# Kernel tuning notes

Hardware: AMD Instinct MI355X
Metric: run time of the kernel (lower is better)

The kernel has to match this reference:

```python
import jax, jax.numpy as jnp
import numpy as np

N_NODES = 50000
N_EDGES = 800000
D = 64
K_ORDER = 8


def setup_inputs() -> dict:
    key = jax.random.key(0)
    k1, k2, k3, k4 = jax.random.split(key, 4)
    x = jax.random.normal(k1, (N_NODES, D), dtype=jnp.float32)
    edge_index = jax.random.randint(k2, (2, N_EDGES), 0, N_NODES, dtype=jnp.int64)
    edge_weight = jax.random.uniform(k3, (N_EDGES,), dtype=jnp.float32)
    weight = jax.random.normal(k4, (K_ORDER, D, D), dtype=jnp.float32) * 0.05
    bias = jnp.zeros((D,), dtype=jnp.float32)
    return {"x": x, "edge_index": edge_index, "edge_weight": edge_weight,
            "weight": weight, "bias": bias}


def _propagate(h, src, dst, edge_weight, n_nodes):
    # sparse matvec: out[i] = sum_{e: dst_e = i} w_e * h[src_e]
    msgs = edge_weight[:, None] * h[src]          # (E, D)
    return jax.ops.segment_sum(msgs, dst, num_segments=n_nodes)


def reference(x, edge_index, edge_weight, weight, bias):
    src, dst = edge_index[0], edge_index[1]
    n = x.shape[0]
    K = weight.shape[0]
    # Chebyshev recursion: T_0 = x, T_1 = L x, T_k = 2 L T_{k-1} - T_{k-2}
    Tx_prev = x                                   # T_0
    out = jnp.einsum('nd,de->ne', Tx_prev, weight[0])
    Tx_cur = _propagate(x, src, dst, edge_weight, n)  # T_1
    if K > 1:
        out = out + jnp.einsum('nd,de->ne', Tx_cur, weight[1])
    for k in range(2, K):
        Tx_next = 2.0 * _propagate(Tx_cur, src, dst, edge_weight, n) - Tx_prev
        out = out + jnp.einsum('nd,de->ne', Tx_next, weight[k])
        Tx_prev, Tx_cur = Tx_cur, Tx_next
    return out + bias
```

## Files before the change

kernel.cpp:

```cpp
#include <hip/hip_runtime.h>
#include <hip/hip_fp16.h>

#define DD  64
#define BKT 256
#define CAP 4608
#define CHK 4096


__device__ __forceinline__ unsigned pk_bf16(float a, float b) {
    unsigned ua = __float_as_uint(a), ub = __float_as_uint(b);
    ua = (ua + 0x7fffu + ((ua >> 16) & 1u)) >> 16;
    ub = (ub + 0x7fffu + ((ub >> 16) & 1u)) & 0xffff0000u;
    return (ua & 0xffffu) | ub;
}
__device__ __forceinline__ void unpk_bf16(unsigned u, float& lo, float& hi) {
    lo = __uint_as_float(u << 16);
    hi = __uint_as_float(u & 0xffff0000u);
}


__global__ __launch_bounds__(256) void p1fill_kernel(
    const int* __restrict__ ei, const float* __restrict__ ew,
    int* __restrict__ bcur, uint2* __restrict__ tmp, int E)
{
    __shared__ int lh[256], gb[256], lc[256];
    int tid = threadIdx.x;
    lh[tid] = 0;
    __syncthreads();
    int base = blockIdx.x * CHK;
#pragma unroll
    for (int j = 0; j < CHK / 256; ++j) {
        int e = base + j * 256 + tid;
        if (e < E) atomicAdd(&lh[ei[E + e] >> 8], 1);
    }
    __syncthreads();
    {
        gb[tid] = lh[tid] ? atomicAdd(&bcur[tid], lh[tid]) : 0;
        lc[tid] = 0;
    }
    __syncthreads();
#pragma unroll
    for (int j = 0; j < CHK / 256; ++j) {
        int e = base + j * 256 + tid;
        if (e < E) {
            int src = ei[e], dst = ei[E + e];
            unsigned short hw = __half_as_ushort(__float2half(ew[e]));
            unsigned rec = (unsigned)(unsigned short)src | ((unsigned)hw << 16);
            int b = dst >> 8;
            int pos = gb[b] + atomicAdd(&lc[b], 1);
            if (pos < CAP)
                tmp[(size_t)b * CAP + pos] = make_uint2(rec, (unsigned)(dst & 255));
        }
    }
}

__global__ __launch_bounds__(256) void p1scan_kernel(
    const int* __restrict__ bcur, int* __restrict__ bptr, int NB, int E)
{
    __shared__ int s[256];
    int t = threadIdx.x;
    int v = (t < NB) ? min(bcur[t], CAP) : 0;
    s[t] = v;
    __syncthreads();
    for (int off = 1; off < 256; off <<= 1) {
        int u = (t >= off) ? s[t - off] : 0;
        __syncthreads();
        s[t] += u;
        __syncthreads();
    }
    if (t < NB) bptr[t] = s[t] - v;
    if (t == 0) bptr[NB] = (NB > 0) ? s[255] : E;
}

__global__ __launch_bounds__(1024) void p2sort_kernel(
    const uint2* __restrict__ tmp, const int* __restrict__ bcur,
    const int* __restrict__ bptr, unsigned* __restrict__ edges,
    int* __restrict__ row_ptr, int N, int E, int NB)
{
    __shared__ int lh[BKT], lx[BKT], lc[BKT];
    __shared__ unsigned lout[CAP];
    int b = blockIdx.x;
    size_t tbase = (size_t)b * CAP;
    int obase = bptr[b];
    int cnt = min(bcur[b], CAP);
    int t = threadIdx.x;
    if (t < BKT) lh[t] = 0;
    __syncthreads();
    for (int i = t; i < cnt; i += 1024)
        atomicAdd(&lh[tmp[tbase + i].y & 255], 1);
    __syncthreads();
    if (t < BKT) { lc[t] = lh[t]; lx[t] = lh[t]; }
    __syncthreads();
    for (int off = 1; off < BKT; off <<= 1) {
        int v = 0;
        if (t < BKT && t >= off) v = lx[t - off];
        __syncthreads();
        if (t < BKT && t >= off) lx[t] += v;
        __syncthreads();
    }
    if (t < BKT) { lx[t] -= lc[t]; lc[t] = 0; }
    __syncthreads();
    for (int i = t; i < cnt; i += 1024) {
        uint2 r = tmp[tbase + i];
        int dl = r.y & 255;
        int pos = lx[dl] + atomicAdd(&lc[dl], 1);
        lout[pos] = r.x;
    }
    __syncthreads();
    for (int i = t; i < cnt; i += 1024) edges[obase + i] = lout[i];
    if (t < BKT) {
        int d = b * BKT + t;
        if (d < N) row_ptr[d] = obase + lx[t];
    }
    if (b == NB - 1 && t == 0) row_ptr[N] = E;
}

__global__ __launch_bounds__(256) void quant_kernel(
    const float4* __restrict__ src, uint4* __restrict__ dst, int n8)
{
    int i = blockIdx.x * 256 + threadIdx.x;
    if (i >= n8) return;
    float4 a = src[2 * i], b = src[2 * i + 1];
    dst[i] = make_uint4(pk_bf16(a.x, a.y), pk_bf16(a.z, a.w),
                        pk_bf16(b.x, b.y), pk_bf16(b.z, b.w));
}

__global__ __launch_bounds__(256) void prop_kernel(
    const unsigned short* __restrict__ h, const unsigned short* __restrict__ prev,
    const unsigned* __restrict__ edges, const int* __restrict__ row_ptr,
    unsigned short* __restrict__ Tnext, int N)
{
    int lane = threadIdx.x & 63;
    int wid  = (blockIdx.x * 256 + threadIdx.x) >> 6;
    int n0 = wid * 2, n1 = n0 + 1;
    if (n0 >= N) return;
    bool v1 = n1 < N;

    int g  = lane >> 3;
    int c8 = (lane & 7) << 3;

    int beg0 = row_ptr[n0];
    int end0 = row_ptr[n0 + 1];
    int beg1 = end0;
    int end1 = v1 ? row_ptr[n1 + 1] : end0;

    float4 A0 = make_float4(0.f, 0.f, 0.f, 0.f), A1 = A0;
    float4 B0 = A0, B1 = A0;

    int b0 = beg0, b1 = beg1;
    while (b0 < end0 || b1 < end1) {
        unsigned RA0 = (b0 + g     < end0) ? __builtin_nontemporal_load(edges + b0 + g)     : 0u;
        unsigned RB0 = (b0 + 8 + g < end0) ? __builtin_nontemporal_load(edges + b0 + 8 + g) : 0u;
        unsigned RA1 = (b1 + g     < end1) ? __builtin_nontemporal_load(edges + b1 + g)     : 0u;
        unsigned RB1 = (b1 + 8 + g < end1) ? __builtin_nontemporal_load(edges + b1 + 8 + g) : 0u;
        float wa0 = __half2float(__ushort_as_half((unsigned short)(RA0 >> 16)));
        float wb0 = __half2float(__ushort_as_half((unsigned short)(RB0 >> 16)));
        float wa1 = __half2float(__ushort_as_half((unsigned short)(RA1 >> 16)));
        float wb1 = __half2float(__ushort_as_half((unsigned short)(RB1 >> 16)));
        const uint4 va0 = *reinterpret_cast<const uint4*>(
            &h[(size_t)(RA0 & 0xffffu) * DD + c8]);
        const uint4 vb0 = *reinterpret_cast<const uint4*>(
            &h[(size_t)(RB0 & 0xffffu) * DD + c8]);
        const uint4 va1 = *reinterpret_cast<const uint4*>(
            &h[(size_t)(RA1 & 0xffffu) * DD + c8]);
        const uint4 vb1 = *reinterpret_cast<const uint4*>(
            &h[(size_t)(RB1 & 0xffffu) * DD + c8]);
        float lo, hi;
        unpk_bf16(va0.x, lo, hi); A0.x = fmaf(wa0, lo, A0.x); A0.y = fmaf(wa0, hi, A0.y);
        unpk_bf16(va0.y, lo, hi); A0.z = fmaf(wa0, lo, A0.z); A0.w = fmaf(wa0, hi, A0.w);
        unpk_bf16(va0.z, lo, hi); A1.x = fmaf(wa0, lo, A1.x); A1.y = fmaf(wa0, hi, A1.y);
        unpk_bf16(va0.w, lo, hi); A1.z = fmaf(wa0, lo, A1.z); A1.w = fmaf(wa0, hi, A1.w);
        unpk_bf16(vb0.x, lo, hi); A0.x = fmaf(wb0, lo, A0.x); A0.y = fmaf(wb0, hi, A0.y);
        unpk_bf16(vb0.y, lo, hi); A0.z = fmaf(wb0, lo, A0.z); A0.w = fmaf(wb0, hi, A0.w);
        unpk_bf16(vb0.z, lo, hi); A1.x = fmaf(wb0, lo, A1.x); A1.y = fmaf(wb0, hi, A1.y);
        unpk_bf16(vb0.w, lo, hi); A1.z = fmaf(wb0, lo, A1.z); A1.w = fmaf(wb0, hi, A1.w);
        unpk_bf16(va1.x, lo, hi); B0.x = fmaf(wa1, lo, B0.x); B0.y = fmaf(wa1, hi, B0.y);
        unpk_bf16(va1.y, lo, hi); B0.z = fmaf(wa1, lo, B0.z); B0.w = fmaf(wa1, hi, B0.w);
        unpk_bf16(va1.z, lo, hi); B1.x = fmaf(wa1, lo, B1.x); B1.y = fmaf(wa1, hi, B1.y);
        unpk_bf16(va1.w, lo, hi); B1.z = fmaf(wa1, lo, B1.z); B1.w = fmaf(wa1, hi, B1.w);
        unpk_bf16(vb1.x, lo, hi); B0.x = fmaf(wb1, lo, B0.x); B0.y = fmaf(wb1, hi, B0.y);
        unpk_bf16(vb1.y, lo, hi); B0.z = fmaf(wb1, lo, B0.z); B0.w = fmaf(wb1, hi, B0.w);
        unpk_bf16(vb1.z, lo, hi); B1.x = fmaf(wb1, lo, B1.x); B1.y = fmaf(wb1, hi, B1.y);
        unpk_bf16(vb1.w, lo, hi); B1.z = fmaf(wb1, lo, B1.z); B1.w = fmaf(wb1, hi, B1.w);
        b0 += 16; b1 += 16;
    }

#pragma unroll
    for (int mk = 8; mk <= 32; mk <<= 1) {
        A0.x += __shfl_xor(A0.x, mk); A0.y += __shfl_xor(A0.y, mk);
        A0.z += __shfl_xor(A0.z, mk); A0.w += __shfl_xor(A0.w, mk);
        A1.x += __shfl_xor(A1.x, mk); A1.y += __shfl_xor(A1.y, mk);
        A1.z += __shfl_xor(A1.z, mk); A1.w += __shfl_xor(A1.w, mk);
        B0.x += __shfl_xor(B0.x, mk); B0.y += __shfl_xor(B0.y, mk);
        B0.z += __shfl_xor(B0.z, mk); B0.w += __shfl_xor(B0.w, mk);
        B1.x += __shfl_xor(B1.x, mk); B1.y += __shfl_xor(B1.y, mk);
        B1.z += __shfl_xor(B1.z, mk); B1.w += __shfl_xor(B1.w, mk);
    }

    if (prev) {
        {
            const uint4 p = *reinterpret_cast<const uint4*>(&prev[(size_t)n0 * DD + c8]);
            float lo, hi;
            unpk_bf16(p.x, lo, hi); A0.x = 2.f * A0.x - lo; A0.y = 2.f * A0.y - hi;
            unpk_bf16(p.y, lo, hi); A0.z = 2.f * A0.z - lo; A0.w = 2.f * A0.w - hi;
            unpk_bf16(p.z, lo, hi); A1.x = 2.f * A1.x - lo; A1.y = 2.f * A1.y - hi;
            unpk_bf16(p.w, lo, hi); A1.z = 2.f * A1.z - lo; A1.w = 2.f * A1.w - hi;
        }
        if (v1) {
            const uint4 p = *reinterpret_cast<const uint4*>(&prev[(size_t)n1 * DD + c8]);
            float lo, hi;
            unpk_bf16(p.x, lo, hi); B0.x = 2.f * B0.x - lo; B0.y = 2.f * B0.y - hi;
            unpk_bf16(p.y, lo, hi); B0.z = 2.f * B0.z - lo; B0.w = 2.f * B0.w - hi;
            unpk_bf16(p.z, lo, hi); B1.x = 2.f * B1.x - lo; B1.y = 2.f * B1.y - hi;
            unpk_bf16(p.w, lo, hi); B1.z = 2.f * B1.z - lo; B1.w = 2.f * B1.w - hi;
        }
    }
    if (g == 0) {
        *reinterpret_cast<uint4*>(&Tnext[(size_t)n0 * DD + c8]) =
            make_uint4(pk_bf16(A0.x, A0.y), pk_bf16(A0.z, A0.w),
                       pk_bf16(A1.x, A1.y), pk_bf16(A1.z, A1.w));
        if (v1)
            *reinterpret_cast<uint4*>(&Tnext[(size_t)n1 * DD + c8]) =
                make_uint4(pk_bf16(B0.x, B0.y), pk_bf16(B0.z, B0.w),
                           pk_bf16(B1.x, B1.y), pk_bf16(B1.z, B1.w));
    }
}

__global__ __launch_bounds__(256) void mega_gemm_kernel(
    const unsigned short* __restrict__ T0, const unsigned short* __restrict__ T1,
    const unsigned short* __restrict__ T2, const unsigned short* __restrict__ T3,
    const float* __restrict__ W, const float* __restrict__ bias,
    float* __restrict__ out, int N, int nord, int init)
{
    __shared__ float Ws[DD * DD];
    __shared__ float Ts[32][68];
    const unsigned short* Tl[4] = { T0, T1, T2, T3 };

    int nb0 = blockIdx.x * 32;
    int tid = threadIdx.x;
    int r = tid >> 4, c = tid & 15;
    int r2 = r * 2, c4 = c * 4;

    float acc[2][4];
    if (init) {
        const float4 bb = *reinterpret_cast<const float4*>(&bias[c4]);
#pragma unroll
        for (int i = 0; i < 2; ++i) {
            acc[i][0] = bb.x; acc[i][1] = bb.y; acc[i][2] = bb.z; acc[i][3] = bb.w;
        }
    } else {
#pragma unroll
        for (int i = 0; i < 2; ++i)
            acc[i][0] = acc[i][1] = acc[i][2] = acc[i][3] = 0.f;
    }

    int nl = tid >> 3, q = tid & 7;
    bool tvalid = (nb0 + nl) < N;

    uint4 tv = make_uint4(0, 0, 0, 0);
    float wv[16];
    if (tvalid)
        tv = *reinterpret_cast<const uint4*>(&Tl[0][(size_t)(nb0 + nl) * DD + q * 8]);
#pragma unroll
    for (int j = 0; j < 16; ++j) wv[j] = W[tid + j * 256];

    for (int kc = 0; kc < nord; ++kc) {
        __syncthreads();
        {
            float f0, f1, f2, f3, f4, f5, f6, f7;
            unpk_bf16(tv.x, f0, f1); unpk_bf16(tv.y, f2, f3);
            unpk_bf16(tv.z, f4, f5); unpk_bf16(tv.w, f6, f7);
            *reinterpret_cast<float4*>(&Ts[nl][q * 8])     = make_float4(f0, f1, f2, f3);
            *reinterpret_cast<float4*>(&Ts[nl][q * 8 + 4]) = make_float4(f4, f5, f6, f7);
#pragma unroll
            for (int j = 0; j < 16; ++j) Ws[tid + j * 256] = wv[j];
        }
        __syncthreads();

        if (kc + 1 < nord) {
            if (tvalid)
                tv = *reinterpret_cast<const uint4*>(
                    &Tl[kc + 1][(size_t)(nb0 + nl) * DD + q * 8]);
            const float* Wn = W + (size_t)(kc + 1) * DD * DD;
#pragma unroll
            for (int j = 0; j < 16; ++j) wv[j] = Wn[tid + j * 256];
        }

#pragma unroll 8
        for (int d = 0; d < DD; ++d) {
            float a0 = Ts[r2 + 0][d], a1 = Ts[r2 + 1][d];
            float4 b = *reinterpret_cast<const float4*>(&Ws[d * DD + c4]);
            acc[0][0] = fmaf(a0, b.x, acc[0][0]); acc[0][1] = fmaf(a0, b.y, acc[0][1]);
            acc[0][2] = fmaf(a0, b.z, acc[0][2]); acc[0][3] = fmaf(a0, b.w, acc[0][3]);
            acc[1][0] = fmaf(a1, b.x, acc[1][0]); acc[1][1] = fmaf(a1, b.y, acc[1][1]);
            acc[1][2] = fmaf(a1, b.z, acc[1][2]); acc[1][3] = fmaf(a1, b.w, acc[1][3]);
        }
    }

#pragma unroll
    for (int i = 0; i < 2; ++i) {
        int n = nb0 + r2 + i;
        if (n < N) {
            float4 o = make_float4(acc[i][0], acc[i][1], acc[i][2], acc[i][3]);
            if (!init) {
                float4 p = *reinterpret_cast<const float4*>(&out[(size_t)n * DD + c4]);
                o.x += p.x; o.y += p.y; o.z += p.z; o.w += p.w;
            }
            *reinterpret_cast<float4*>(&out[(size_t)n * DD + c4]) = o;
        }
    }
}


static inline size_t rup(size_t x) { return (x + 255) & ~(size_t)255; }

extern "C" void kernel_launch(void* const* d_in, const int* in_sizes, int n_in,
                              void* d_out, int out_size, void* d_ws, size_t ws_size,
                              hipStream_t stream) {
    const float* x    = (const float*)d_in[0];
    const int*   ei   = (const int*)  d_in[1];
    const float* ew   = (const float*)d_in[2];
    const float* W    = (const float*)d_in[3];
    const float* bias = (const float*)d_in[4];
    float* out = (float*)d_out;

    int N = in_sizes[0] / DD;
    int E = in_sizes[2];
    int K = in_sizes[3] / (DD * DD);
    int NB = (N + BKT - 1) / BKT;

    size_t nb_bf = (size_t)N * DD * sizeof(unsigned short);

    char* w = (char*)d_ws;
    unsigned short* B[5];
    for (int i = 0; i < 5; ++i) { B[i] = (unsigned short*)w; w += rup(nb_bf); }
    unsigned* edges  = (unsigned*)w;  w += rup((size_t)E * sizeof(unsigned));
    int* row_ptr = (int*)w;           w += rup((size_t)(N + 1) * sizeof(int));
    int* bptr    = (int*)w;           w += rup((size_t)(NB + 1) * sizeof(int));
    int* bcur    = (int*)w;           w += rup((size_t)NB * sizeof(int));
    uint2* tmp   = (uint2*)B[1];

    int pb   = (N + 7) / 8;
    int gb32 = (N + 31) / 32;
    int n8   = (N * DD) / 8;
    int qb   = (n8 + 255) / 256;
    int fb   = (E + CHK - 1) / CHK;

    hipMemsetAsync(bcur, 0, (size_t)NB * sizeof(int), stream);
    p1fill_kernel<<<fb, 256, 0, stream>>>(ei, ew, bcur, tmp, E);
    p1scan_kernel<<<1, 256, 0, stream>>>(bcur, bptr, NB, E);
    p2sort_kernel<<<NB, 1024, 0, stream>>>(tmp, bcur, bptr, edges, row_ptr, N, E, NB);

    quant_kernel<<<qb, 256, 0, stream>>>((const float4*)x, (uint4*)B[0], n8);

    int done = 0;
    for (int k = 1; k < K; ++k) {
        const unsigned short* cur  = B[(k - 1) % 5];
        const unsigned short* prev = (k >= 2) ? B[(k - 2) % 5] : nullptr;
        unsigned short*       nxt  = B[k % 5];
        prop_kernel<<<pb, 256, 0, stream>>>(cur, prev, edges, row_ptr, nxt, N);
        if (k % 4 == 3) {
            int c0 = done;
            mega_gemm_kernel<<<gb32, 256, 0, stream>>>(
                B[(c0 + 0) % 5], B[(c0 + 1) % 5], B[(c0 + 2) % 5], B[(c0 + 3) % 5],
                W + (size_t)c0 * DD * DD, bias, out, N, 4, done == 0);
            done += 4;
        }
    }
    if (done < K) {
        mega_gemm_kernel<<<gb32, 256, 0, stream>>>(
            B[(done + 0) % 5], B[(done + 1) % 5],
            B[(done + 2) % 5], B[(done + 3) % 5],
            W + (size_t)done * DD * DD, bias, out, N, K - done, done == 0);
    }
}
```

Measured before the change: 255.0 us.

## Replace FP32 FMA Chebyshev GEMM with bf16 MFMA using split hi/lo weights

Rewrites the fused per-order output GEMM to use 16x16x32 bf16 MFMA instructions instead of scalar FP32 FMAs over shared-memory tiles. Each block now handles 64 nodes, one 16-row tile per wavefront. The bf16 activations are fed directly from global memory as the A operand. Weights are split in shared memory into bf16 high and low parts, each multiplied separately, to keep near-FP32 weight precision. The change cuts ALU and LDS traffic in the GEMM stage. In exchange it doubles the MFMA count, re-converts the weights in every block for every order, and reads the last partial tile without a bounds check.

Measured after the change: 234.7 us. 8.0% less time.

```diff
diff --git a/kernel.cpp b/kernel.cpp
--- a/kernel.cpp
+++ b/kernel.cpp
@@ -5,6 +5,9 @@
 #define BKT 256
 #define CAP 4608
 #define CHK 4096
+
+typedef __attribute__((ext_vector_type(8))) short bf16x8;
+typedef __attribute__((ext_vector_type(4))) float f32x4;
 
 
 __device__ __forceinline__ unsigned pk_bf16(float a, float b) {
@@ -16,6 +19,13 @@
 __device__ __forceinline__ void unpk_bf16(unsigned u, float& lo, float& hi) {
     lo = __uint_as_float(u << 16);
     hi = __uint_as_float(u & 0xffff0000u);
+}
+__device__ __forceinline__ unsigned short bf16_rtn(float f) {
+    unsigned u = __float_as_uint(f);
+    return (unsigned short)((u + 0x7fffu + ((u >> 16) & 1u)) >> 16);
+}
+__device__ __forceinline__ float bf16_to_f(unsigned short h) {
+    return __uint_as_float((unsigned)h << 16);
 }
 
 
@@ -226,87 +236,74 @@
     }
 }
 
-__global__ __launch_bounds__(256) void mega_gemm_kernel(
+__global__ __launch_bounds__(256) void mega_mfma_kernel(
     const unsigned short* __restrict__ T0, const unsigned short* __restrict__ T1,
     const unsigned short* __restrict__ T2, const unsigned short* __restrict__ T3,
     const float* __restrict__ W, const float* __restrict__ bias,
     float* __restrict__ out, int N, int nord, int init)
 {
-    __shared__ float Ws[DD * DD];
-    __shared__ float Ts[32][68];
+    __shared__ unsigned short WtHi[64][72];
+    __shared__ unsigned short WtLo[64][72];
     const unsigned short* Tl[4] = { T0, T1, T2, T3 };
 
-    int nb0 = blockIdx.x * 32;
-    int tid = threadIdx.x;
-    int r = tid >> 4, c = tid & 15;
-    int r2 = r * 2, c4 = c * 4;
-
-    float acc[2][4];
-    if (init) {
-        const float4 bb = *reinterpret_cast<const float4*>(&bias[c4]);
-#pragma unroll
-        for (int i = 0; i < 2; ++i) {
-            acc[i][0] = bb.x; acc[i][1] = bb.y; acc[i][2] = bb.z; acc[i][3] = bb.w;
-        }
-    } else {
-#pragma unroll
-        for (int i = 0; i < 2; ++i)
-            acc[i][0] = acc[i][1] = acc[i][2] = acc[i][3] = 0.f;
-    }
-
-    int nl = tid >> 3, q = tid & 7;
-    bool tvalid = (nb0 + nl) < N;
-
-    uint4 tv = make_uint4(0, 0, 0, 0);
-    float wv[16];
-    if (tvalid)
-        tv = *reinterpret_cast<const uint4*>(&Tl[0][(size_t)(nb0 + nl) * DD + q * 8]);
-#pragma unroll
-    for (int j = 0; j < 16; ++j) wv[j] = W[tid + j * 256];
+    int tid  = threadIdx.x;
+    int lane = tid & 63;
+    int wv   = tid >> 6;
+    int nb0  = blockIdx.x * 64;
+    int l15  = lane & 15;
+    int lg   = lane >> 4;
+
+    f32x4 acc[4];
+#pragma unroll
+    for (int t = 0; t < 4; ++t) acc[t] = (f32x4){0.f, 0.f, 0.f, 0.f};
 
     for (int kc = 0; kc < nord; ++kc) {
         __syncthreads();
         {
-            float f0, f1, f2, f3, f4, f5, f6, f7;
-            unpk_bf16(tv.x, f0, f1); unpk_bf16(tv.y, f2, f3);
-            unpk_bf16(tv.z, f4, f5); unpk_bf16(tv.w, f6, f7);
-            *reinterpret_cast<float4*>(&Ts[nl][q * 8])     = make_float4(f0, f1, f2, f3);
-            *reinterpret_cast<float4*>(&Ts[nl][q * 8 + 4]) = make_float4(f4, f5, f6, f7);
-#pragma unroll
-            for (int j = 0; j < 16; ++j) Ws[tid + j * 256] = wv[j];
-        }
-        __syncthreads();
-
-        if (kc + 1 < nord) {
-            if (tvalid)
-                tv = *reinterpret_cast<const uint4*>(
-                    &Tl[kc + 1][(size_t)(nb0 + nl) * DD + q * 8]);
-            const float* Wn = W + (size_t)(kc + 1) * DD * DD;
-#pragma unroll
-            for (int j = 0; j < 16; ++j) wv[j] = Wn[tid + j * 256];
-        }
-
-#pragma unroll 8
-        for (int d = 0; d < DD; ++d) {
-            float a0 = Ts[r2 + 0][d], a1 = Ts[r2 + 1][d];
-            float4 b = *reinterpret_cast<const float4*>(&Ws[d * DD + c4]);
-            acc[0][0] = fmaf(a0, b.x, acc[0][0]); acc[0][1] = fmaf(a0, b.y, acc[0][1]);
-            acc[0][2] = fmaf(a0, b.z, acc[0][2]); acc[0][3] = fmaf(a0, b.w, acc[0][3]);
-            acc[1][0] = fmaf(a1, b.x, acc[1][0]); acc[1][1] = fmaf(a1, b.y, acc[1][1]);
-            acc[1][2] = fmaf(a1, b.z, acc[1][2]); acc[1][3] = fmaf(a1, b.w, acc[1][3]);
-        }
-    }
-
-#pragma unroll
-    for (int i = 0; i < 2; ++i) {
-        int n = nb0 + r2 + i;
-        if (n < N) {
-            float4 o = make_float4(acc[i][0], acc[i][1], acc[i][2], acc[i][3]);
-            if (!init) {
-                float4 p = *reinterpret_cast<const float4*>(&out[(size_t)n * DD + c4]);
-                o.x += p.x; o.y += p.y; o.z += p.z; o.w += p.w;
+            const float* Wk = W + (size_t)kc * DD * DD;
+            int d = tid >> 2, c0 = (tid & 3) * 16;
+#pragma unroll
+            for (int j = 0; j < 16; ++j) {
+                float w = Wk[d * DD + c0 + j];
+                unsigned short hi = bf16_rtn(w);
+                unsigned short lo = bf16_rtn(w - bf16_to_f(hi));
+                WtHi[c0 + j][d] = hi;
+                WtLo[c0 + j][d] = lo;
             }
-            *reinterpret_cast<float4*>(&out[(size_t)n * DD + c4]) = o;
+        }
+        __syncthreads();
+
+        const unsigned short* Tk = Tl[kc];
+        size_t abase = (size_t)(nb0 + wv * 16 + l15) * DD + lg * 8;
+        bf16x8 a0 = *reinterpret_cast<const bf16x8*>(&Tk[abase]);
+        bf16x8 a1 = *reinterpret_cast<const bf16x8*>(&Tk[abase + 32]);
+
+#pragma unroll
+        for (int kch = 0; kch < 2; ++kch) {
+            bf16x8 a = kch ? a1 : a0;
+            int kb = kch * 32 + lg * 8;
+#pragma unroll
+            for (int t = 0; t < 4; ++t) {
+                bf16x8 bhi = *reinterpret_cast<const bf16x8*>(&WtHi[t * 16 + l15][kb]);
+                bf16x8 blo = *reinterpret_cast<const bf16x8*>(&WtLo[t * 16 + l15][kb]);
+                acc[t] = __builtin_amdgcn_mfma_f32_16x16x32_bf16(a, bhi, acc[t], 0, 0, 0);
+                acc[t] = __builtin_amdgcn_mfma_f32_16x16x32_bf16(a, blo, acc[t], 0, 0, 0);
+            }
+        }
+    }
+
+#pragma unroll
+    for (int t = 0; t < 4; ++t) {
+        int col = t * 16 + l15;
+        float bv = init ? bias[col] : 0.f;
+#pragma unroll
+        for (int j = 0; j < 4; ++j) {
+            int n = nb0 + wv * 16 + lg * 4 + j;
+            if (n < N) {
+                float v = acc[t][j] + bv;
+                if (!init) v += out[(size_t)n * DD + col];
+                out[(size_t)n * DD + col] = v;
+            }
         }
     }
 }
@@ -341,7 +338,7 @@
     uint2* tmp   = (uint2*)B[1];
 
     int pb   = (N + 7) / 8;
-    int gb32 = (N + 31) / 32;
+    int gb64 = (N + 63) / 64;
     int n8   = (N * DD) / 8;
     int qb   = (n8 + 255) / 256;
     int fb   = (E + CHK - 1) / CHK;
@@ -361,14 +358,14 @@
         prop_kernel<<<pb, 256, 0, stream>>>(cur, prev, edges, row_ptr, nxt, N);
         if (k % 4 == 3) {
             int c0 = done;
-            mega_gemm_kernel<<<gb32, 256, 0, stream>>>(
+            mega_mfma_kernel<<<gb64, 256, 0, stream>>>(
                 B[(c0 + 0) % 5], B[(c0 + 1) % 5], B[(c0 + 2) % 5], B[(c0 + 3) % 5],
                 W + (size_t)c0 * DD * DD, bias, out, N, 4, done == 0);
             done += 4;
         }
     }
     if (done < K) {
-        mega_gemm_kernel<<<gb32, 256, 0, stream>>>(
+        mega_mfma_kernel<<<gb64, 256, 0, stream>>>(
             B[(done + 0) % 5], B[(done + 1) % 5],
             B[(done + 2) % 5], B[(done + 3) % 5],
             W + (size_t)done * DD * DD, bias, out, N, K - done, done == 0);
```
